# Optimization experiments

Measured on AMD Instinct MI355X. Metric: run time of the kernel, lower is better.

Reference implementation:

```python
import jax, jax.numpy as jnp
import numpy as np

N, E, G = 10000, 40000, 64   # nodes, edges, graphs
ED, H, OUT = 4, 64, 4        # edge_attr_dim, hidden, output_dim


def _nnconv(x, src, dst, edge_attr, w1, b1, w2, b2, root_w, bias, in_dim, out_dim, n_nodes):
    # edge MLP: Linear -> ReLU -> Linear, producing per-edge [in_dim, out_dim] weights
    h = jax.nn.relu(edge_attr @ w1 + b1) @ w2 + b2        # [E, in*out]
    W = h.reshape(-1, in_dim, out_dim)                    # [E, in, out]
    msg = jnp.einsum('ei,eio->eo', x[src], W)             # gather + per-edge matmul
    s = jax.ops.segment_sum(msg, dst, num_segments=n_nodes)
    cnt = jax.ops.segment_sum(jnp.ones((msg.shape[0],), x.dtype), dst, num_segments=n_nodes)
    agg = s / jnp.maximum(cnt, 1.0)[:, None]              # scatter-mean (0 for isolated nodes)
    return agg + x @ root_w + bias                        # NNConv root weight + bias


def setup_inputs():
    key = jax.random.key(0)
    ks = jax.random.split(key, 16)
    lin = lambda k, i, o: jax.random.normal(k, (i, o), jnp.float32) * 0.05
    inp = {}
    inp['node_ids'] = jax.random.normal(ks[0], (N, 1), jnp.float32)
    inp['edge_index'] = jax.random.randint(ks[1], (2, E), 0, N)
    inp['edge_attr'] = jax.random.normal(ks[2], (E, ED), jnp.float32)
    inp['batch'] = jnp.sort(jax.random.randint(ks[3], (N,), 0, G))
    # layer 0: in=1, out=H
    inp['w1_0'] = lin(ks[4], ED, 1 * H); inp['b1_0'] = jnp.zeros((1 * H,), jnp.float32)
    inp['w2_0'] = lin(ks[5], 1 * H, 1 * H); inp['b2_0'] = jnp.zeros((1 * H,), jnp.float32)
    inp['root_0'] = lin(ks[6], 1, H); inp['bias_0'] = jnp.zeros((H,), jnp.float32)
    # layer 1: in=H, out=H
    inp['w1_1'] = lin(ks[7], ED, H * H); inp['b1_1'] = jnp.zeros((H * H,), jnp.float32)
    inp['w2_1'] = lin(ks[8], H * H, H * H); inp['b2_1'] = jnp.zeros((H * H,), jnp.float32)
    inp['root_1'] = lin(ks[9], H, H); inp['bias_1'] = jnp.zeros((H,), jnp.float32)
    # classifier
    inp['wc1'] = lin(ks[10], H, H); inp['bc1'] = jnp.zeros((H,), jnp.float32)
    inp['wc2'] = lin(ks[11], H, OUT); inp['bc2'] = jnp.zeros((OUT,), jnp.float32)
    return inp


def reference(node_ids, edge_index, edge_attr, batch,
              w1_0, b1_0, w2_0, b2_0, root_0, bias_0,
              w1_1, b1_1, w2_1, b2_1, root_1, bias_1,
              wc1, bc1, wc2, bc2):
    src, dst = edge_index[0], edge_index[1]
    x = node_ids
    x = jax.nn.relu(_nnconv(x, src, dst, edge_attr, w1_0, b1_0, w2_0, b2_0, root_0, bias_0, 1, H, N))
    x = jax.nn.relu(_nnconv(x, src, dst, edge_attr, w1_1, b1_1, w2_1, b2_1, root_1, bias_1, H, H, N))
    # dropout omitted (inference mode)
    gs = jax.ops.segment_sum(x, batch, num_segments=G)
    gc = jax.ops.segment_sum(jnp.ones((N,), x.dtype), batch, num_segments=G)
    pooled = gs / jnp.maximum(gc, 1.0)[:, None]           # global_mean_pool
    h = jax.nn.relu(pooled @ wc1 + bc1)
    return h @ wc2 + bc2
```

## Files before the change

### kernel.cpp

```cpp
#include <hip/hip_runtime.h>
#include <hip/hip_fp16.h>

#define N_NODES 10000
#define N_EDGES 40000
#define N_GRAPH 64
#define CPS     258
#define NTILES  1256
#define EPAD    40192
#define PSLICE  (EPAD * 64)

typedef _Float16 half8_t  __attribute__((ext_vector_type(8)));
typedef float    floatx16 __attribute__((ext_vector_type(16)));

__device__ __forceinline__ void gload_lds16(const void* g, void* l) {
  __builtin_amdgcn_global_load_lds((const __attribute__((address_space(1))) void*)g,
                                   (__attribute__((address_space(3))) void*)l, 16, 0, 0);
}

__device__ __host__ __forceinline__ int swz(int row) {
  return ((row & 3) << 1) | ((row >> 2) & 1);
}

__device__ __forceinline__ half8_t splat8(_Float16 v) {
  half8_t r = {v, v, v, v, v, v, v, v};
  return r;
}

union U32H2 { unsigned int u; __half2 h2; };

__global__ void prep_B(const float* __restrict__ w2, const float* __restrict__ b2,
                       _Float16* __restrict__ BC) {
  int tid = blockIdx.x * 256 + threadIdx.x;
  if (tid >= 8 * CPS * 64) return;
  int ks  = tid / (CPS * 64);
  int rem = tid - ks * (CPS * 64);
  int c = rem >> 6;
  int o = rem & 63;
  _Float16* dst = BC + (size_t)tid * 128;
  if (c > 256 || (c == 256 && ks != 7)) {
    for (int j = 0; j < 128; ++j) dst[j] = (_Float16)0.f;
    return;
  }
  int swo = swz(o);
  int kkbase = ks * 32768 + c * 128;
  for (int sp = 0; sp < 16; ++sp) {
    int kk0 = kkbase + ((sp ^ swo) * 8);
    #pragma unroll
    for (int j3 = 0; j3 < 8; ++j3) {
      int kk_l = kk0 + j3;
      int k = kk_l >> 6, i = kk_l & 63;
      float v;
      if (k < 4096)       v = w2[k * 4096 + i * 64 + o];
      else if (k == 4096) v = b2[i * 64 + o];
      else                v = 0.f;
      dst[sp * 8 + j3] = (_Float16)v;
    }
  }
}

__global__ void prep_W(const float* __restrict__ w1, const float* __restrict__ b1,
                       unsigned int* __restrict__ WP) {
  int tid = blockIdx.x * 256 + threadIdx.x;
  if (tid >= 8 * 256) return;
  int ks = tid >> 8, c = tid & 255;
  int kb = ks * 512 + 2 * c;
  unsigned int* dst = WP + (size_t)tid * 8;
  #pragma unroll
  for (int d = 0; d < 4; ++d) {
    float2 v = *(const float2*)(w1 + d * 4096 + kb);
    U32H2 u; u.h2 = __floats2half2_rn(v.x, v.y);
    dst[d] = u.u;
  }
  float2 bv = *(const float2*)(b1 + kb);
  U32H2 u; u.h2 = __floats2half2_rn(bv.x, bv.y);
  dst[4] = u.u; dst[5] = 0; dst[6] = 0; dst[7] = 0;
}

__global__ void layer0_edge(const float* __restrict__ node_ids,
                            const int* __restrict__ ei,
                            const float* __restrict__ ea,
                            const float* __restrict__ w1, const float* __restrict__ b1,
                            const float* __restrict__ w2, const float* __restrict__ b2,
                            float* __restrict__ agg0, float* __restrict__ cnt) {
  __shared__ float w1s[256], b1s[64], w2s[4096], b2s[64], zb[4][64];
  int t = threadIdx.x;
  for (int idx = t; idx < 4096; idx += 256) w2s[idx] = w2[idx];
  if (t < 256) w1s[t] = w1[t];
  if (t < 64) { b1s[t] = b1[t]; b2s[t] = b2[t]; }
  __syncthreads();
  int w = t >> 6, l = t & 63;
  int gw = blockIdx.x * 4 + w;
  int nw = gridDim.x * 4;
  for (int e = gw; e < N_EDGES; e += nw) {
    float a0 = ea[e * 4 + 0], a1 = ea[e * 4 + 1], a2 = ea[e * 4 + 2], a3 = ea[e * 4 + 3];
    float z = a0 * w1s[l] + a1 * w1s[64 + l] + a2 * w1s[128 + l] + a3 * w1s[192 + l] + b1s[l];
    zb[w][l] = fmaxf(z, 0.f);
    asm volatile("s_waitcnt lgkmcnt(0)" ::: "memory");
    __builtin_amdgcn_sched_barrier(0);
    float h = b2s[l];
    #pragma unroll
    for (int k = 0; k < 64; ++k) h += zb[w][k] * w2s[k * 64 + l];
    int src = ei[e], dst = ei[N_EDGES + e];
    float msg = node_ids[src] * h;
    atomicAdd(&agg0[dst * 64 + l], msg);
    if (l == 0) atomicAdd(&cnt[dst], 1.0f);
  }
}

__global__ void node0(const float* __restrict__ node_ids, const int* __restrict__ batch,
                      const float* __restrict__ agg0, const float* __restrict__ cnt,
                      const float* __restrict__ root0, const float* __restrict__ bias0,
                      float* __restrict__ x1, float* __restrict__ pcnt) {
  int gid = blockIdx.x * 256 + threadIdx.x;
  if (gid >= N_NODES * 64) return;
  int n = gid >> 6, o = gid & 63;
  float c = fmaxf(cnt[n], 1.f);
  float v = agg0[gid] / c + node_ids[n] * root0[o] + bias0[o];
  x1[gid] = fmaxf(v, 0.f);
  if (o == 0) atomicAdd(&pcnt[batch[n]], 1.0f);
}

template <bool PART>
__launch_bounds__(256, 3)
__global__ void fused_edge_gemm(const int* __restrict__ ei,
                                const float* __restrict__ ea,
                                const float* __restrict__ x1,
                                const unsigned int* __restrict__ WP,
                                const _Float16* __restrict__ BC,
                                float* __restrict__ outbuf) {
  __shared__ __attribute__((aligned(16))) _Float16 Bl[3][64 * 128];
  int t = threadIdx.x;
  int ks = blockIdx.x & 7;
  int eb = blockIdx.x >> 3;
  int e0 = eb * 256;
  int w = t >> 6, l = t & 63;
  int half_ = l >> 5;
  int lane31 = l & 31;
  int swo = swz(lane31);

  half8_t xh8[2][4];
  __half2 eb_bc[2][4];
  #pragma unroll
  for (int m = 0; m < 2; ++m) {
    int e = e0 + w * 64 + m * 32 + lane31;
    if (e < N_EDGES) {
      int src = ei[e];
      const float* xp = x1 + src * 64 + half_ * 8;
      #pragma unroll
      for (int q = 0; q < 4; ++q) {
        float4 f0 = *(const float4*)(xp + q * 16);
        float4 f1 = *(const float4*)(xp + q * 16 + 4);
        half8_t v;
        v[0] = (_Float16)f0.x; v[1] = (_Float16)f0.y;
        v[2] = (_Float16)f0.z; v[3] = (_Float16)f0.w;
        v[4] = (_Float16)f1.x; v[5] = (_Float16)f1.y;
        v[6] = (_Float16)f1.z; v[7] = (_Float16)f1.w;
        xh8[m][q] = v;
      }
      float4 av = *(const float4*)(ea + e * 4);
      eb_bc[m][0] = __float2half2_rn(av.x); eb_bc[m][1] = __float2half2_rn(av.y);
      eb_bc[m][2] = __float2half2_rn(av.z); eb_bc[m][3] = __float2half2_rn(av.w);
    } else {
      #pragma unroll
      for (int q = 0; q < 4; ++q) xh8[m][q] = splat8((_Float16)0.f);
      #pragma unroll
      for (int d = 0; d < 4; ++d) eb_bc[m][d] = __float2half2_rn(0.f);
    }
  }

  floatx16 acc[2][2];
  #pragma unroll
  for (int m = 0; m < 2; ++m)
    #pragma unroll
    for (int n = 0; n < 2; ++n)
      #pragma unroll
      for (int r = 0; r < 16; ++r) acc[m][n][r] = 0.f;

  const char* gp = (const char*)BC + (size_t)ks * (CPS * 16384) + w * 4096 + l * 16;
  char*       sd = (char*)&Bl[0][0] + w * 4096 + l * 16;
  const char* rb = (const char*)&Bl[0][0] + lane31 * 256;
  const unsigned int* wp = WP + (size_t)ks * 256 * 8;

  auto stg = [&](int sb) {
    char* d = sd + sb * 16384;
    gload_lds16(gp,        d);
    gload_lds16(gp + 1024, d + 1024);
    gload_lds16(gp + 2048, d + 2048);
    gload_lds16(gp + 3072, d + 3072);
    gp += 16384;
  };

  const __half zero1 = __float2half(0.f);
  union H2F { __half2 h2; _Float16 f[2]; };
  half8_t zs8[2][2];

  auto zgen = [&](int c) {
    uint4 wv = *(const uint4*)(wp + c * 8);
    unsigned int bb = wp[c * 8 + 4];
    U32H2 uw0, uw1, uw2, uw3, ub;
    uw0.u = wv.x; uw1.u = wv.y; uw2.u = wv.z; uw3.u = wv.w; ub.u = bb;
    #pragma unroll
    for (int m = 0; m < 2; ++m) {
      __half2 h = __hfma2(eb_bc[m][0], uw0.h2, ub.h2);
      h = __hfma2(eb_bc[m][1], uw1.h2, h);
      h = __hfma2(eb_bc[m][2], uw2.h2, h);
      h = __hfma2(eb_bc[m][3], uw3.h2, h);
      H2F u; u.h2 = __halves2half2(__hmax(__low2half(h),  zero1),
                                   __hmax(__high2half(h), zero1));
      zs8[m][0] = splat8(u.f[0]);
      zs8[m][1] = splat8(u.f[1]);
    }
  };
  auto zbias = [&]() {
    #pragma unroll
    for (int m = 0; m < 2; ++m) {
      zs8[m][0] = splat8((_Float16)1.f);
      zs8[m][1] = splat8((_Float16)0.f);
    }
  };

  auto cmp = [&](int rbuf) {
    const char* base = rb + rbuf * 16384;
    __builtin_amdgcn_s_setprio(1);
    #pragma unroll
    for (int t8 = 0; t8 < 8; ++t8) {
      int slot = (t8 * 2 + half_) ^ swo;
      const char* ba = base + slot * 16;
      half8_t bf0 = *(const half8_t*)ba;
      half8_t bf1 = *(const half8_t*)(ba + 8192);
      #pragma unroll
      for (int m = 0; m < 2; ++m) {
        half8_t af = xh8[m][t8 & 3] * zs8[m][t8 >> 2];
        acc[m][0] = __builtin_amdgcn_mfma_f32_32x32x16_f16(af, bf0, acc[m][0], 0, 0, 0);
        acc[m][1] = __builtin_amdgcn_mfma_f32_32x32x16_f16(af, bf1, acc[m][1], 0, 0, 0);
      }
    }
    __builtin_amdgcn_s_setprio(0);
  };

#define SYNC4 do { asm volatile("s_waitcnt vmcnt(4)" ::: "memory"); \
                   __builtin_amdgcn_sched_barrier(0); \
                   __builtin_amdgcn_s_barrier(); \
                   __builtin_amdgcn_sched_barrier(0); } while (0)
#define SYNC0 do { asm volatile("s_waitcnt vmcnt(0)" ::: "memory"); \
                   __builtin_amdgcn_sched_barrier(0); \
                   __builtin_amdgcn_s_barrier(); \
                   __builtin_amdgcn_sched_barrier(0); } while (0)

  stg(0); stg(1);

  int c = 0;
  for (int it = 0; it < 85; ++it) {
    zgen(c);     SYNC4; stg(2); cmp(0);
    zgen(c + 1); SYNC4; stg(0); cmp(1);
    zgen(c + 2); SYNC4; stg(1); cmp(2);
    c += 3;
  }
  zgen(255); SYNC4; stg(2); cmp(0);
  zbias();   SYNC4;         cmp(1);
  zbias();   SYNC0;         cmp(2);

#undef SYNC4
#undef SYNC0

  if (PART) {
    float* pb = outbuf + ((size_t)ks * EPAD + e0 + w * 64) * 64 + lane31;
    #pragma unroll
    for (int m = 0; m < 2; ++m) {
      #pragma unroll
      for (int r = 0; r < 16; ++r) {
        int row = m * 32 + (r & 3) + 8 * (r >> 2) + 4 * half_;
        pb[(size_t)row * 64]      = acc[m][0][r];
        pb[(size_t)row * 64 + 32] = acc[m][1][r];
      }
    }
  } else {
    #pragma unroll
    for (int m = 0; m < 2; ++m) {
      #pragma unroll
      for (int r = 0; r < 16; ++r) {
        int e = e0 + w * 64 + m * 32 + (r & 3) + 8 * (r >> 2) + 4 * half_;
        if (e < N_EDGES) {
          int dst = ei[N_EDGES + e];
          atomicAdd(&outbuf[dst * 64 + lane31],      acc[m][0][r]);
          atomicAdd(&outbuf[dst * 64 + lane31 + 32], acc[m][1][r]);
        }
      }
    }
  }
}

__global__ void reduce_partials(const float* __restrict__ P8, const int* __restrict__ ei,
                                float* __restrict__ agg1) {
  int gid = blockIdx.x * 256 + threadIdx.x;
  if (gid >= N_EDGES * 64) return;
  int e = gid >> 6;
  float s = 0.f;
  #pragma unroll
  for (int ks = 0; ks < 8; ++ks) s += P8[(size_t)ks * PSLICE + gid];
  int dst = ei[N_EDGES + e];
  atomicAdd(&agg1[dst * 64 + (gid & 63)], s);
}

__global__ void node1_pool(const int* __restrict__ batch, const float* __restrict__ x1,
                           const float* __restrict__ agg1, const float* __restrict__ cnt,
                           const float* __restrict__ root1, const float* __restrict__ bias1,
                           float* __restrict__ psum) {
  __shared__ float rt[4096];
  int t = threadIdx.x;
  for (int idx = t; idx < 4096; idx += 256) rt[idx] = root1[idx];
  __syncthreads();
  int w = t >> 6, l = t & 63;
  int n = blockIdx.x * 4 + w;
  if (n >= N_NODES) return;
  float c = fmaxf(cnt[n], 1.f);
  float acc = agg1[n * 64 + l] / c + bias1[l];
  const float* xp = x1 + n * 64;
  #pragma unroll
  for (int i4 = 0; i4 < 16; ++i4) {
    float4 xv = *(const float4*)(xp + i4 * 4);
    acc += xv.x * rt[(i4 * 4 + 0) * 64 + l] + xv.y * rt[(i4 * 4 + 1) * 64 + l]
         + xv.z * rt[(i4 * 4 + 2) * 64 + l] + xv.w * rt[(i4 * 4 + 3) * 64 + l];
  }
  acc = fmaxf(acc, 0.f);
  atomicAdd(&psum[batch[n] * 64 + l], acc);
}

__global__ void classifier(const float* __restrict__ psum, const float* __restrict__ pcnt,
                           const float* __restrict__ wc1, const float* __restrict__ bc1,
                           const float* __restrict__ wc2, const float* __restrict__ bc2,
                           float* __restrict__ out) {
  __shared__ float hb[64];
  int g = blockIdx.x, j = threadIdx.x;
  float c = fmaxf(pcnt[g], 1.f);
  float h = bc1[j];
  const float* pp = psum + g * 64;
  #pragma unroll
  for (int i4 = 0; i4 < 16; ++i4) {
    float4 pv = *(const float4*)(pp + i4 * 4);
    h += (pv.x / c) * wc1[(i4 * 4 + 0) * 64 + j] + (pv.y / c) * wc1[(i4 * 4 + 1) * 64 + j]
       + (pv.z / c) * wc1[(i4 * 4 + 2) * 64 + j] + (pv.w / c) * wc1[(i4 * 4 + 3) * 64 + j];
  }
  hb[j] = fmaxf(h, 0.f);
  __syncthreads();
  if (j < 4) {
    float o = bc2[j];
    #pragma unroll
    for (int k = 0; k < 64; ++k) o += hb[k] * wc2[k * 4 + j];
    out[g * 4 + j] = o;
  }
}

extern "C" void kernel_launch(void* const* d_in, const int* in_sizes, int n_in,
                              void* d_out, int out_size, void* d_ws, size_t ws_size,
                              hipStream_t stream) {
  const float* node_ids = (const float*)d_in[0];
  const int*   ei       = (const int*)d_in[1];
  const float* ea       = (const float*)d_in[2];
  const int*   batch    = (const int*)d_in[3];
  const float* w1_0 = (const float*)d_in[4];
  const float* b1_0 = (const float*)d_in[5];
  const float* w2_0 = (const float*)d_in[6];
  const float* b2_0 = (const float*)d_in[7];
  const float* root0 = (const float*)d_in[8];
  const float* bias0 = (const float*)d_in[9];
  const float* w1_1 = (const float*)d_in[10];
  const float* b1_1 = (const float*)d_in[11];
  const float* w2_1 = (const float*)d_in[12];
  const float* b2_1 = (const float*)d_in[13];
  const float* root1 = (const float*)d_in[14];
  const float* bias1 = (const float*)d_in[15];
  const float* wc1 = (const float*)d_in[16];
  const float* bc1 = (const float*)d_in[17];
  const float* wc2 = (const float*)d_in[18];
  const float* bc2 = (const float*)d_in[19];
  float* out = (float*)d_out;

  char* ws = (char*)d_ws;
  _Float16* BC = (_Float16*)ws;
  unsigned int* WP = (unsigned int*)(ws + 33816576);
  float* x1   = (float*)(ws + 33882112);
  float* agg0 = (float*)(ws + 36442112);
  float* agg1 = (float*)(ws + 39002112);
  float* cnt  = (float*)(ws + 41562112);
  float* psum = (float*)(ws + 41602112);
  float* pcnt = (float*)(ws + 41618496);
  float* P8   = (float*)(ws + 41618752);
  const size_t NEED_PART = 41618752ull + (size_t)8 * PSLICE * 4;

  (void)hipMemsetAsync(agg0, 0, 2560000 + 2560000 + 40000 + 16384 + 256, stream);

  prep_B<<<(8 * CPS * 64 + 255) / 256, 256, 0, stream>>>(w2_1, b2_1, BC);
  prep_W<<<8, 256, 0, stream>>>(w1_1, b1_1, WP);
  layer0_edge<<<512, 256, 0, stream>>>(node_ids, ei, ea, w1_0, b1_0, w2_0, b2_0, agg0, cnt);
  node0<<<(N_NODES * 64 + 255) / 256, 256, 0, stream>>>(node_ids, batch, agg0, cnt, root0, bias0, x1, pcnt);

  if (ws_size >= NEED_PART) {
    fused_edge_gemm<true><<<NTILES, 256, 0, stream>>>(ei, ea, x1, WP, BC, P8);
    reduce_partials<<<(N_EDGES * 64) / 256, 256, 0, stream>>>(P8, ei, agg1);
  } else {
    fused_edge_gemm<false><<<NTILES, 256, 0, stream>>>(ei, ea, x1, WP, BC, agg1);
  }

  node1_pool<<<(N_NODES + 3) / 4, 256, 0, stream>>>(batch, x1, agg1, cnt, root1, bias1, psum);
  classifier<<<N_GRAPH, 64, 0, stream>>>(psum, pcnt, wc1, bc1, wc2, bc2, out);
}
```

Before: 1.391 ms.

## Split warps 2x2 over edges and output cols; coalesce prep_B reads

The fused edge GEMM now arranges its four warps as a 2x2 grid. Each warp covers 128 edges and 32 output columns instead of 64 edges and all 64 columns, so it loads one B fragment per step and reuses it across four MFMA row tiles. That halves LDS B reads per MFMA, but doubles the per-thread work of building the A operand (x gather and z generation) and raises register pressure with 4x4 xh8. prep_B is also rewritten so each thread handles one k position across all 64 outputs, which makes the w2 reads contiguous instead of strided.

```diff
diff --git a/kernel.cpp b/kernel.cpp
--- a/kernel.cpp
+++ b/kernel.cpp
@@ -31,30 +31,30 @@
 __global__ void prep_B(const float* __restrict__ w2, const float* __restrict__ b2,
                        _Float16* __restrict__ BC) {
   int tid = blockIdx.x * 256 + threadIdx.x;
-  if (tid >= 8 * CPS * 64) return;
-  int ks  = tid / (CPS * 64);
-  int rem = tid - ks * (CPS * 64);
-  int c = rem >> 6;
-  int o = rem & 63;
-  _Float16* dst = BC + (size_t)tid * 128;
-  if (c > 256 || (c == 256 && ks != 7)) {
-    for (int j = 0; j < 128; ++j) dst[j] = (_Float16)0.f;
-    return;
-  }
-  int swo = swz(o);
-  int kkbase = ks * 32768 + c * 128;
-  for (int sp = 0; sp < 16; ++sp) {
-    int kk0 = kkbase + ((sp ^ swo) * 8);
-    #pragma unroll
-    for (int j3 = 0; j3 < 8; ++j3) {
-      int kk_l = kk0 + j3;
-      int k = kk_l >> 6, i = kk_l & 63;
-      float v;
-      if (k < 4096)       v = w2[k * 4096 + i * 64 + o];
-      else if (k == 4096) v = b2[i * 64 + o];
-      else                v = 0.f;
-      dst[sp * 8 + j3] = (_Float16)v;
-    }
+  if (tid >= 8 * CPS * 128) return;
+  int ks  = tid / (CPS * 128);
+  int rem = tid - ks * (CPS * 128);
+  int c   = rem >> 7;
+  int pos = rem & 127;
+  int sl = pos >> 3, j3 = pos & 7;
+  _Float16* dstb = BC + ((size_t)(ks * CPS + c) * 64) * 128;
+  bool pad = (c > 256) || (c == 256 && ks != 7);
+  int kk_l = ks * 32768 + c * 128 + pos;
+  int k = kk_l >> 6, i = kk_l & 63;
+  if (pad || k > 4096) {
+    #pragma unroll 8
+    for (int o = 0; o < 64; ++o)
+      dstb[o * 128 + ((sl ^ swz(o)) << 3) + j3] = (_Float16)0.f;
+  } else if (k < 4096) {
+    const float* src = w2 + (size_t)k * 4096 + i * 64;
+    #pragma unroll 8
+    for (int o = 0; o < 64; ++o)
+      dstb[o * 128 + ((sl ^ swz(o)) << 3) + j3] = (_Float16)src[o];
+  } else {
+    const float* src = b2 + i * 64;
+    #pragma unroll 8
+    for (int o = 0; o < 64; ++o)
+      dstb[o * 128 + ((sl ^ swz(o)) << 3) + j3] = (_Float16)src[o];
   }
 }
 
@@ -136,13 +136,15 @@
   int w = t >> 6, l = t & 63;
   int half_ = l >> 5;
   int lane31 = l & 31;
+  int wr = w >> 1;
+  int wc = w & 1;
   int swo = swz(lane31);
 
-  half8_t xh8[2][4];
-  __half2 eb_bc[2][4];
-  #pragma unroll
-  for (int m = 0; m < 2; ++m) {
-    int e = e0 + w * 64 + m * 32 + lane31;
+  half8_t xh8[4][4];
+  __half2 ea01[4], ea23[4];
+  #pragma unroll
+  for (int m = 0; m < 4; ++m) {
+    int e = e0 + wr * 128 + m * 32 + lane31;
     if (e < N_EDGES) {
       int src = ei[e];
       const float* xp = x1 + src * 64 + half_ * 8;
@@ -158,27 +160,25 @@
         xh8[m][q] = v;
       }
       float4 av = *(const float4*)(ea + e * 4);
-      eb_bc[m][0] = __float2half2_rn(av.x); eb_bc[m][1] = __float2half2_rn(av.y);
-      eb_bc[m][2] = __float2half2_rn(av.z); eb_bc[m][3] = __float2half2_rn(av.w);
+      ea01[m] = __floats2half2_rn(av.x, av.y);
+      ea23[m] = __floats2half2_rn(av.z, av.w);
     } else {
       #pragma unroll
       for (int q = 0; q < 4; ++q) xh8[m][q] = splat8((_Float16)0.f);
-      #pragma unroll
-      for (int d = 0; d < 4; ++d) eb_bc[m][d] = __float2half2_rn(0.f);
-    }
-  }
-
-  floatx16 acc[2][2];
-  #pragma unroll
-  for (int m = 0; m < 2; ++m)
-    #pragma unroll
-    for (int n = 0; n < 2; ++n)
-      #pragma unroll
-      for (int r = 0; r < 16; ++r) acc[m][n][r] = 0.f;
+      ea01[m] = __floats2half2_rn(0.f, 0.f);
+      ea23[m] = __floats2half2_rn(0.f, 0.f);
+    }
+  }
+
+  floatx16 acc[4];
+  #pragma unroll
+  for (int m = 0; m < 4; ++m)
+    #pragma unroll
+    for (int r = 0; r < 16; ++r) acc[m][r] = 0.f;
 
   const char* gp = (const char*)BC + (size_t)ks * (CPS * 16384) + w * 4096 + l * 16;
   char*       sd = (char*)&Bl[0][0] + w * 4096 + l * 16;
-  const char* rb = (const char*)&Bl[0][0] + lane31 * 256;
+  const char* rb = (const char*)&Bl[0][0] + (wc * 32 + lane31) * 256;
   const unsigned int* wp = WP + (size_t)ks * 256 * 8;
 
   auto stg = [&](int sb) {
@@ -192,7 +192,7 @@
 
   const __half zero1 = __float2half(0.f);
   union H2F { __half2 h2; _Float16 f[2]; };
-  half8_t zs8[2][2];
+  half8_t zs8[4][2];
 
   auto zgen = [&](int c) {
     uint4 wv = *(const uint4*)(wp + c * 8);
@@ -200,11 +200,11 @@
     U32H2 uw0, uw1, uw2, uw3, ub;
     uw0.u = wv.x; uw1.u = wv.y; uw2.u = wv.z; uw3.u = wv.w; ub.u = bb;
     #pragma unroll
-    for (int m = 0; m < 2; ++m) {
-      __half2 h = __hfma2(eb_bc[m][0], uw0.h2, ub.h2);
-      h = __hfma2(eb_bc[m][1], uw1.h2, h);
-      h = __hfma2(eb_bc[m][2], uw2.h2, h);
-      h = __hfma2(eb_bc[m][3], uw3.h2, h);
+    for (int m = 0; m < 4; ++m) {
+      __half2 h = __hfma2(__half2half2(__low2half(ea01[m])),  uw0.h2, ub.h2);
+      h = __hfma2(__half2half2(__high2half(ea01[m])), uw1.h2, h);
+      h = __hfma2(__half2half2(__low2half(ea23[m])),  uw2.h2, h);
+      h = __hfma2(__half2half2(__high2half(ea23[m])), uw3.h2, h);
       H2F u; u.h2 = __halves2half2(__hmax(__low2half(h),  zero1),
                                    __hmax(__high2half(h), zero1));
       zs8[m][0] = splat8(u.f[0]);
@@ -213,7 +213,7 @@
   };
   auto zbias = [&]() {
     #pragma unroll
-    for (int m = 0; m < 2; ++m) {
+    for (int m = 0; m < 4; ++m) {
       zs8[m][0] = splat8((_Float16)1.f);
       zs8[m][1] = splat8((_Float16)0.f);
     }
@@ -225,14 +225,11 @@
     #pragma unroll
     for (int t8 = 0; t8 < 8; ++t8) {
       int slot = (t8 * 2 + half_) ^ swo;
-      const char* ba = base + slot * 16;
-      half8_t bf0 = *(const half8_t*)ba;
-      half8_t bf1 = *(const half8_t*)(ba + 8192);
+      half8_t bf = *(const half8_t*)(base + slot * 16);
       #pragma unroll
-      for (int m = 0; m < 2; ++m) {
+      for (int m = 0; m < 4; ++m) {
         half8_t af = xh8[m][t8 & 3] * zs8[m][t8 >> 2];
-        acc[m][0] = __builtin_amdgcn_mfma_f32_32x32x16_f16(af, bf0, acc[m][0], 0, 0, 0);
-        acc[m][1] = __builtin_amdgcn_mfma_f32_32x32x16_f16(af, bf1, acc[m][1], 0, 0, 0);
+        acc[m] = __builtin_amdgcn_mfma_f32_32x32x16_f16(af, bf, acc[m], 0, 0, 0);
       }
     }
     __builtin_amdgcn_s_setprio(0);
@@ -264,26 +261,24 @@
 #undef SYNC0
 
   if (PART) {
-    float* pb = outbuf + ((size_t)ks * EPAD + e0 + w * 64) * 64 + lane31;
-    #pragma unroll
-    for (int m = 0; m < 2; ++m) {
+    float* pb = outbuf + ((size_t)ks * EPAD + e0 + wr * 128) * 64 + wc * 32 + lane31;
+    #pragma unroll
+    for (int m = 0; m < 4; ++m) {
       #pragma unroll
       for (int r = 0; r < 16; ++r) {
         int row = m * 32 + (r & 3) + 8 * (r >> 2) + 4 * half_;
-        pb[(size_t)row * 64]      = acc[m][0][r];
-        pb[(size_t)row * 64 + 32] = acc[m][1][r];
+        pb[(size_t)row * 64] = acc[m][r];
       }
     }
   } else {
     #pragma unroll
-    for (int m = 0; m < 2; ++m) {
+    for (int m = 0; m < 4; ++m) {
       #pragma unroll
       for (int r = 0; r < 16; ++r) {
-        int e = e0 + w * 64 + m * 32 + (r & 3) + 8 * (r >> 2) + 4 * half_;
+        int e = e0 + wr * 128 + m * 32 + (r & 3) + 8 * (r >> 2) + 4 * half_;
         if (e < N_EDGES) {
           int dst = ei[N_EDGES + e];
-          atomicAdd(&outbuf[dst * 64 + lane31],      acc[m][0][r]);
-          atomicAdd(&outbuf[dst * 64 + lane31 + 32], acc[m][1][r]);
+          atomicAdd(&outbuf[dst * 64 + wc * 32 + lane31], acc[m][r]);
         }
       }
     }
@@ -390,7 +385,7 @@
 
   (void)hipMemsetAsync(agg0, 0, 2560000 + 2560000 + 40000 + 16384 + 256, stream);
 
-  prep_B<<<(8 * CPS * 64 + 255) / 256, 256, 0, stream>>>(w2_1, b2_1, BC);
+  prep_B<<<(8 * CPS * 128 + 255) / 256, 256, 0, stream>>>(w2_1, b2_1, BC);
   prep_W<<<8, 256, 0, stream>>>(w1_1, b1_1, WP);
   layer0_edge<<<512, 256, 0, stream>>>(node_ids, ei, ea, w1_0, b1_0, w2_0, b2_0, agg0, cnt);
   node0<<<(N_NODES * 64 + 255) / 256, 256, 0, stream>>>(node_ids, batch, agg0, cnt, root0, bias0, x1, pcnt);
```

Result: faster. 1.346 ms (-3.3%).
